# Optimization experiments

Hardware: AMD Instinct MI355X
Metric: run time of the kernel (lower is better)

The kernel has to match this reference:

```python
import jax, jax.numpy as jnp
import numpy as np
from jax import lax

WIN_SIZE = 11
SIGMA = 1.5
WEIGHTS = jnp.array([0.0448, 0.2856, 0.3001, 0.2363, 0.1333], dtype=jnp.float32)
C1 = (0.01 * 1.0) ** 2  # val_range = 1.0
C2 = (0.03 * 1.0) ** 2


def gaussian_kernel2d(kernel_size, sigma):
    g = jnp.arange(kernel_size, dtype=jnp.float32) - kernel_size // 2
    g = jnp.exp(-(g ** 2) / (2.0 * sigma ** 2))
    g = g / g.sum()
    return jnp.outer(g, g)  # [k, k]


def depthwise_conv(x, k2d):
    # x: [B, C, H, W]; same gaussian window applied per-channel (groups=C), VALID padding
    C = x.shape[1]
    w = jnp.broadcast_to(k2d, (C, 1) + k2d.shape).astype(x.dtype)
    return lax.conv_general_dilated(x, w, (1, 1), 'VALID',
                                    feature_group_count=C,
                                    dimension_numbers=('NCHW', 'OIHW', 'NCHW'))


def ssim_index(x, y, k2d, nonnegative=True):
    # returns (ss, cs) each of shape [B, C] (spatial mean, per channel)
    m1 = depthwise_conv(x, k2d)
    m2 = depthwise_conv(y, k2d)
    m12 = m1 * m2
    m1s = m1 * m1
    m2s = m2 * m2
    v1 = depthwise_conv(x * x, k2d) - m1s
    v2 = depthwise_conv(y * y, k2d) - m2s
    cov = depthwise_conv(x * y, k2d) - m12
    cs = (2.0 * cov + C2) / (v1 + v2 + C2)
    ss = (2.0 * m12 + C1) / (m1s + m2s + C1) * cs
    ss = ss.reshape(ss.shape[0], ss.shape[1], -1).mean(axis=-1)
    cs = cs.reshape(cs.shape[0], cs.shape[1], -1).mean(axis=-1)
    if nonnegative:
        ss = jnp.maximum(ss, 0.0)
        cs = jnp.maximum(cs, 0.0)
    return ss, cs


def avg_pool2(x):
    # F.avg_pool2d(kernel_size=2). Input spatial dims are even at every scale
    # (512 -> 32), so ceil_mode never pads; plain 2x2/2 mean pooling is exact.
    s = lax.reduce_window(x, jnp.array(0.0, x.dtype), lax.add,
                          (1, 1, 2, 2), (1, 1, 2, 2), 'VALID')
    return s * 0.25


def setup_inputs() -> dict:
    key = jax.random.key(0)
    k1, k2 = jax.random.split(key)
    B, C, H, W = 4, 12, 512, 512
    pred = jax.random.normal(k1, (B, C, H, W), dtype=jnp.float32)
    target = jax.random.randint(k2, (B, H, W), 0, C, dtype=jnp.int64)
    return {"pred": pred, "target": target}


def reference(pred, target):
    # MS_SSIMLoss.forward with process_input=True, nonnegative=True.
    # The per-class python loop in the original is an independent depthwise
    # computation per channel -> vectorized here as a C-channel grouped conv;
    # loss = mean over classes of (1 - mean over batch of msss) == 1 - mean(msss).
    num_classes = pred.shape[1]
    x = jax.nn.softmax(pred, axis=1)
    y = jax.nn.one_hot(target, num_classes, dtype=pred.dtype).transpose(0, 3, 1, 2)
    k2d = gaussian_kernel2d(WIN_SIZE, SIGMA)
    m = WEIGHTS.shape[0]
    vals = []
    for i in range(m):
        if i > 0:
            x = avg_pool2(x)
            y = avg_pool2(y)
        ss, cs = ssim_index(x, y, k2d, nonnegative=True)
        vals.append(cs if i + 1 < m else ss)
    stacked = jnp.stack(vals, axis=-1)  # [B, C, m]
    msss = jnp.prod(stacked ** WEIGHTS, axis=-1)  # [B, C]
    return 1.0 - msss.mean()
```

## Files before the change

### kernel.cpp

```cpp
#include <hip/hip_runtime.h>

#define NCH 12
#define NB  4
#define BC  48
#define HW0 (512 * 512)

#define GK_INIT { 0.00102840f, 0.00759863f, 0.03600078f, 0.10936081f, \
                  0.21300541f, 0.26601164f, 0.21300541f, 0.10936081f, \
                  0.03600078f, 0.00759863f, 0.00102840f }

__global__ void k_denom(const float4* __restrict__ pred, float4* __restrict__ U,
                        double* __restrict__ acc) {
    if (blockIdx.x == 0) {
        for (int t = threadIdx.x; t < 480; t += 256) acc[t] = 0.0;
    }
    int i = blockIdx.x * blockDim.x + threadIdx.x;
    if (i >= NB * (HW0 / 4)) return;
    int b = i >> 16;
    int p = i & 65535;
    const float4* base = pred + (((size_t)b * NCH) << 16) + p;
    float4 s = make_float4(0.f, 0.f, 0.f, 0.f);
#pragma unroll
    for (int c = 0; c < NCH; ++c) {
        float4 v = base[(size_t)c << 16];
        s.x += expf(v.x); s.y += expf(v.y);
        s.z += expf(v.z); s.w += expf(v.w);
    }
    float4 u;
    u.x = 1.f / s.x; u.y = 1.f / s.y; u.z = 1.f / s.z; u.w = 1.f / s.w;
    U[((size_t)b << 16) + p] = u;
}

__global__ __launch_bounds__(256, 8)
void k_ssim0(const float* __restrict__ pred, const float* __restrict__ U,
             const int* __restrict__ tgt, double* __restrict__ acc,
             float* __restrict__ Xp, unsigned short* __restrict__ Yp) {
    constexpr int SS = 43;
    constexpr int TS = 35;
    constexpr int H = 512, W = 512, OH = 502, OW = 502, tilesX = 16;
    __shared__ float sx[42 * SS + 4];
    __shared__ uint2 tm4[42 * TS];
    __shared__ unsigned long long ybits[30];
    __shared__ float red[8];

    const float gk[11] = GK_INIT;

    const int bc = blockIdx.y;
    const int tile = blockIdx.x;
    const int ty = tile / tilesX, tx = tile - ty * tilesX;
    const int oy = ty * 32, ox = tx * 32;
    const int tid = threadIdx.x;
    const bool interior = (oy + 41 < H) && (ox + 41 < W);

    const int b = bc / NCH, cls = bc - (bc / NCH) * NCH;
    const float* Pb = pred + (((size_t)b * NCH + cls) << 18);
    const float* Ub = U + ((size_t)b << 18);
    const int* Tb = tgt + ((size_t)b << 18);

    {
        int r = tid / 42, c = tid - (tid / 42) * 42;
#pragma unroll
        for (int k = 0; k < 7; ++k) {
            bool inr = (k < 6) || (tid < 228);
            int gy = oy + r, gx = ox + c;
            bool ld = inr && (interior || (gy < H && gx < W));
            float xv = 0.f;
            bool bit = false;
            if (ld) {
                int off = gy * W + gx;
                xv = expf(Pb[off]) * Ub[off];
                bit = (Tb[off] == cls);
            }
            unsigned long long mk = __ballot(bit);
            if ((tid & 63) == 0) ybits[(tid >> 6) + (k << 2)] = mk;
            if (inr) sx[r * SS + c] = xv;
            c += 4; r += 6;
            if (c >= 42) { c -= 42; r += 1; }
        }
        if (tid == 0) { ybits[28] = 0ull; ybits[29] = 0ull; }
    }
    __syncthreads();

    if (tid < 252) {
        int rr = tid / 6, s = tid - (tid / 6) * 6;
        int c0 = s * 6;
        const float* px = sx + rr * SS + c0;
        float ac0[6] = {}, ac1[6] = {}, ac2[6] = {}, ac3[6] = {};
        unsigned long long win;
        {
            int i0 = rr * 42 + c0;
            int w = i0 >> 6, sh = i0 & 63;
            unsigned long long lo = ybits[w], hi = ybits[w + 1];
            win = sh ? ((lo >> sh) | (hi << (64 - sh))) : lo;
        }
#pragma unroll
        for (int j = 0; j < 16; ++j) {
            float xv = px[j];
            float xx = xv * xv;
            bool bit = (win >> j) & 1;
            float yv = bit ? 1.f : 0.f;
            float xy = bit ? xv : 0.f;
#pragma unroll
            for (int o = 0; o < 6; ++o) {
                int kk = j - o;
                if (kk >= 0 && kk <= 10) {
                    float g = gk[kk];
                    ac0[o] = fmaf(g, xv, ac0[o]);
                    ac1[o] = fmaf(g, yv, ac1[o]);
                    ac2[o] = fmaf(g, xx, ac2[o]);
                    ac3[o] = fmaf(g, xy, ac3[o]);
                }
            }
        }
        int ob = rr * TS + c0;
#pragma unroll
        for (int o = 0; o < 6; ++o) {
            if (c0 + o < 32) {
                unsigned ua = __float_as_uint(ac0[o]);
                unsigned ub = __float_as_uint(ac1[o]);
                unsigned uc = __float_as_uint(ac2[o]);
                unsigned ud = __float_as_uint(ac3[o]);
                tm4[ob + o] = make_uint2((ua >> 16) | (ub & 0xFFFF0000u),
                                         (uc >> 16) | (ud & 0xFFFF0000u));
            }
        }
    }
    __syncthreads();

    const float C1 = 1e-4f, C2 = 9e-4f;
    const int cc = tid & 31, rg = tid >> 5, r0 = rg << 2;
    float a0[4] = {}, a1[4] = {}, a2[4] = {}, a3[4] = {};
    const int vb = r0 * TS + cc;
#pragma unroll
    for (int k = 0; k < 14; ++k) {
        uint2 tv = tm4[vb + k * TS];
        float m1v = __uint_as_float(tv.x << 16);
        float m2v = __uint_as_float(tv.x & 0xFFFF0000u);
        float xxv = __uint_as_float(tv.y << 16);
        float xyv = __uint_as_float(tv.y & 0xFFFF0000u);
#pragma unroll
        for (int j = 0; j < 4; ++j) {
            int kk = k - j;
            if (kk >= 0 && kk <= 10) {
                float g = gk[kk];
                a0[j] = fmaf(g, m1v, a0[j]);
                a1[j] = fmaf(g, m2v, a1[j]);
                a2[j] = fmaf(g, xxv, a2[j]);
                a3[j] = fmaf(g, xyv, a3[j]);
            }
        }
    }
    float cs_l = 0.f, ss_l = 0.f;
    const bool colok = (ox + cc < OW);
#pragma unroll
    for (int j = 0; j < 4; ++j) {
        if (colok && (oy + r0 + j < OH)) {
            float m1 = a0[j], m2 = a1[j];
            float sxx = a2[j], sxy_ = a3[j];
            float m11 = m1 * m1, m22 = m2 * m2, m12 = m1 * m2;
            float v1 = sxx - m11, v2 = m2 - m22, cov = sxy_ - m12;
            float d1 = m11 + m22 + C1, d2 = v1 + v2 + C2;
            float n2 = 2.f * cov + C2;
            float q = 1.f / (d1 * d2);
            cs_l = fmaf(n2 * d1, q, cs_l);
            ss_l = fmaf((2.f * m12 + C1) * n2, q, ss_l);
        }
    }

    {
        int py = tid >> 4, pxx = tid & 15;
        int s0 = (py * 2) * SS + pxx * 2;
        float xs = 0.25f * (sx[s0] + sx[s0 + 1] + sx[s0 + SS] + sx[s0 + SS + 1]);
        size_t oidx = ((size_t)bc * 256 + (oy >> 1) + py) * 256 + (ox >> 1) + pxx;
        Xp[oidx] = xs;
        int i0 = (py * 2) * 42 + pxx * 2, i1 = i0 + 42;
        unsigned c0 = (unsigned)((ybits[i0 >> 6] >> (i0 & 63)) & 1ull);
        unsigned c1 = (unsigned)((ybits[(i0 + 1) >> 6] >> ((i0 + 1) & 63)) & 1ull);
        unsigned c2 = (unsigned)((ybits[i1 >> 6] >> (i1 & 63)) & 1ull);
        unsigned c3 = (unsigned)((ybits[(i1 + 1) >> 6] >> ((i1 + 1) & 63)) & 1ull);
        Yp[oidx] = (unsigned short)((c0 + c1 + c2 + c3) << 6);
    }

    for (int off = 32; off; off >>= 1) {
        cs_l += __shfl_down(cs_l, off);
        ss_l += __shfl_down(ss_l, off);
    }
    int wv = tid >> 6, ln = tid & 63;
    if (ln == 0) { red[wv] = cs_l; red[4 + wv] = ss_l; }
    __syncthreads();
    if (tid == 0) {
        double cs_b = (double)red[0] + (double)red[1] + (double)red[2] + (double)red[3];
        double ss_b = (double)red[4] + (double)red[5] + (double)red[6] + (double)red[7];
        atomicAdd(&acc[bc], cs_b);
        atomicAdd(&acc[48 + bc], ss_b);
    }
}

template <int PIN>
__device__ __forceinline__ void ssim_tile_g(
    const float* __restrict__ Xs, const unsigned short* __restrict__ Ys,
    int H, int W, int OH, int OW, int tilesX, int tile, int bc,
    double* __restrict__ acc, int scale,
    float* sx, float4* tm4, float* tm5, unsigned short* syu, float* red) {
    constexpr int SS = 43;
    constexpr int TS = 35;
    const float gk[11] = GK_INIT;

    const int ty = tile / tilesX, tx = tile - ty * tilesX;
    const int oy = ty * 32, ox = tx * 32;
    const int tid = threadIdx.x;
    const bool interior = (oy + 41 < H) && (ox + 41 < W);

    constexpr int SC = 1 << PIN;
    const int SW = W * SC;
    const float* Xb = Xs + (size_t)bc * H * W * SC * SC;
    const unsigned short* Yb = Ys + (size_t)bc * H * W * SC * SC;

    {
        int r = tid / 42, c = tid - (tid / 42) * 42;
#pragma unroll
        for (int k = 0; k < 7; ++k) {
            bool inr = (k < 6) || (tid < 228);
            int gy = oy + r, gx = ox + c;
            bool ld = inr && (interior || (gy < H && gx < W));
            float xv = 0.f;
            unsigned short yv = 0;
            if (ld) {
                if constexpr (PIN == 0) {
                    int off = gy * SW + gx;
                    xv = Xb[off];
                    yv = Yb[off];
                } else {
                    const float* q = Xb + (SC * gy) * SW + SC * gx;
                    const unsigned short* qy = Yb + (SC * gy) * SW + SC * gx;
                    float s = 0.f; unsigned us = 0;
#pragma unroll
                    for (int a = 0; a < SC; ++a) {
#pragma unroll
                        for (int e = 0; e < SC; ++e) {
                            s += q[a * SW + e];
                            us += qy[a * SW + e];
                        }
                    }
                    xv = s * (1.f / (float)(SC * SC));
                    yv = (unsigned short)(us >> (2 * PIN));
                }
            }
            if (inr) { sx[r * SS + c] = xv; syu[r * SS + c] = yv; }
            c += 4; r += 6;
            if (c >= 42) { c -= 42; r += 1; }
        }
    }
    __syncthreads();

    if (tid < 252) {
        int rr = tid / 6, s = tid - (tid / 6) * 6;
        int c0 = s * 6;
        const float* px = sx + rr * SS + c0;
        const unsigned short* pyu = syu + rr * SS + c0;
        float ac0[6] = {}, ac1[6] = {}, ac2[6] = {}, ac3[6] = {}, ac4[6] = {};
#pragma unroll
        for (int j = 0; j < 16; ++j) {
            float xv = px[j];
            float xx = xv * xv;
            float yv = (float)pyu[j];
            float xy = xv * yv;
            float yy = yv * yv;
#pragma unroll
            for (int o = 0; o < 6; ++o) {
                int kk = j - o;
                if (kk >= 0 && kk <= 10) {
                    float g = gk[kk];
                    ac0[o] = fmaf(g, xv, ac0[o]);
                    ac1[o] = fmaf(g, yv, ac1[o]);
                    ac2[o] = fmaf(g, xx, ac2[o]);
                    ac3[o] = fmaf(g, xy, ac3[o]);
                    ac4[o] = fmaf(g, yy, ac4[o]);
                }
            }
        }
        int ob = rr * TS + c0;
#pragma unroll
        for (int o = 0; o < 6; ++o) {
            if (c0 + o < 32) {
                tm4[ob + o] = make_float4(ac0[o], ac1[o], ac2[o], ac3[o]);
                tm5[ob + o] = ac4[o];
            }
        }
    }
    __syncthreads();

    const float C1 = 1e-4f, C2 = 9e-4f;
    const int cc = tid & 31, rg = tid >> 5, r0 = rg << 2;
    float a0[4] = {}, a1[4] = {}, a2[4] = {}, a3[4] = {}, a4[4] = {};
    const int vb = r0 * TS + cc;
#pragma unroll
    for (int k = 0; k < 14; ++k) {
        float4 tv = tm4[vb + k * TS];
        float t4 = tm5[vb + k * TS];
#pragma unroll
        for (int j = 0; j < 4; ++j) {
            int kk = k - j;
            if (kk >= 0 && kk <= 10) {
                float g = gk[kk];
                a0[j] = fmaf(g, tv.x, a0[j]);
                a1[j] = fmaf(g, tv.y, a1[j]);
                a2[j] = fmaf(g, tv.z, a2[j]);
                a3[j] = fmaf(g, tv.w, a3[j]);
                a4[j] = fmaf(g, t4, a4[j]);
            }
        }
    }
    float cs_l = 0.f, ss_l = 0.f;
    const bool colok = (ox + cc < OW);
#pragma unroll
    for (int j = 0; j < 4; ++j) {
        if (colok && (oy + r0 + j < OH)) {
            float m1 = a0[j];
            float m2 = a1[j] * (1.f / 256.f);
            float sxx = a2[j];
            float sxy_ = a3[j] * (1.f / 256.f);
            float syy_ = a4[j] * (1.f / 65536.f);
            float m11 = m1 * m1, m22 = m2 * m2, m12 = m1 * m2;
            float v1 = sxx - m11, v2 = syy_ - m22, cov = sxy_ - m12;
            float d1 = m11 + m22 + C1, d2 = v1 + v2 + C2;
            float n2 = 2.f * cov + C2;
            float q = 1.f / (d1 * d2);
            cs_l = fmaf(n2 * d1, q, cs_l);
            ss_l = fmaf((2.f * m12 + C1) * n2, q, ss_l);
        }
    }

    for (int offs = 32; offs; offs >>= 1) {
        cs_l += __shfl_down(cs_l, offs);
        ss_l += __shfl_down(ss_l, offs);
    }
    int wv = tid >> 6, ln = tid & 63;
    if (ln == 0) { red[wv] = cs_l; red[4 + wv] = ss_l; }
    __syncthreads();
    if (tid == 0) {
        double cs_b = (double)red[0] + (double)red[1] + (double)red[2] + (double)red[3];
        double ss_b = (double)red[4] + (double)red[5] + (double)red[6] + (double)red[7];
        atomicAdd(&acc[scale * 96 + bc], cs_b);
        atomicAdd(&acc[scale * 96 + 48 + bc], ss_b);
    }
}

__global__ __launch_bounds__(256, 4)
void k_rest(const float* __restrict__ X1, const unsigned short* __restrict__ Y1,
            double* __restrict__ acc) {
    __shared__ float sx[42 * 43 + 4];
    __shared__ float4 tm4[42 * 35];
    __shared__ float tm5[42 * 35];
    __shared__ unsigned short syu[42 * 43 + 4];
    __shared__ float red[8];
    const int gb = blockIdx.x;

    if (gb < 3072) {
        ssim_tile_g<0>(X1, Y1, 256, 256, 246, 246, 8, gb & 63, gb >> 6,
                       acc, 1, sx, tm4, tm5, syu, red);
    } else if (gb < 3840) {
        int t = gb - 3072;
        ssim_tile_g<1>(X1, Y1, 128, 128, 118, 118, 4, t & 15, t >> 4,
                       acc, 2, sx, tm4, tm5, syu, red);
    } else if (gb < 4032) {
        int t = gb - 3840;
        ssim_tile_g<2>(X1, Y1, 64, 64, 54, 54, 2, t & 3, t >> 2,
                       acc, 3, sx, tm4, tm5, syu, red);
    } else {
        ssim_tile_g<3>(X1, Y1, 32, 32, 22, 22, 1, 0, gb - 4032,
                       acc, 4, sx, tm4, tm5, syu, red);
    }
}

__global__ void k_final(const double* __restrict__ acc, float* __restrict__ out) {
    const float wts[5] = {0.0448f, 0.2856f, 0.3001f, 0.2363f, 0.1333f};
    const float cnt[5] = {252004.f, 60516.f, 13924.f, 2916.f, 484.f};
    int tid = threadIdx.x;
    float msss = 0.f;
    if (tid < BC) {
        msss = 1.f;
#pragma unroll
        for (int s = 0; s < 5; ++s) {
            double a = (s < 4) ? acc[s * 96 + tid] : acc[s * 96 + 48 + tid];
            float v = fmaxf((float)(a / (double)cnt[s]), 0.f);
            msss *= powf(v, wts[s]);
        }
    }
    for (int off = 32; off; off >>= 1) msss += __shfl_down(msss, off);
    if (tid == 0) out[0] = 1.f - msss * (1.f / (float)BC);
}

extern "C" void kernel_launch(void* const* d_in, const int* in_sizes, int n_in,
                              void* d_out, int out_size, void* d_ws, size_t ws_size,
                              hipStream_t stream) {
    const float* pred = (const float*)d_in[0];
    const int*   tgt  = (const int*)d_in[1];
    float* out = (float*)d_out;

    double* acc = (double*)d_ws;
    float* U  = (float*)(acc + 480);
    float* X1 = U + (size_t)NB * 512 * 512;
    unsigned short* Y1 = (unsigned short*)(X1 + (size_t)BC * 256 * 256);

    k_denom<<<(NB * (HW0 / 4) + 255) / 256, 256, 0, stream>>>(
        (const float4*)pred, (float4*)U, acc);

    k_ssim0<<<dim3(256, BC), 256, 0, stream>>>(pred, U, tgt, acc, X1, Y1);

    k_rest<<<dim3(4080), 256, 0, stream>>>(X1, Y1, acc);

    k_final<<<1, 64, 0, stream>>>(acc, out);
}
```

Baseline: 251.8 us.

## Store horizontal-pass intermediates as truncated bf16 in shared memory, use fast exp

The horizontal Gaussian pass results in k_rest are truncated to their upper 16 bits (bf16) and packed, which shrinks the LDS intermediate arrays so more blocks fit per CU (launch bounds raised to 6 waves-per-block occupancy). expf is replaced by __expf in the softmax kernels. Truncating the intermediates loses precision in the variance and covariance terms, where a small difference is taken between two nearly equal values. That could push the SSIM results past tolerance.

```diff
diff --git a/kernel.cpp b/kernel.cpp
--- a/kernel.cpp
+++ b/kernel.cpp
@@ -23,8 +23,8 @@
 #pragma unroll
     for (int c = 0; c < NCH; ++c) {
         float4 v = base[(size_t)c << 16];
-        s.x += expf(v.x); s.y += expf(v.y);
-        s.z += expf(v.z); s.w += expf(v.w);
+        s.x += __expf(v.x); s.y += __expf(v.y);
+        s.z += __expf(v.z); s.w += __expf(v.w);
     }
     float4 u;
     u.x = 1.f / s.x; u.y = 1.f / s.y; u.z = 1.f / s.z; u.w = 1.f / s.w;
@@ -68,7 +68,7 @@
             bool bit = false;
             if (ld) {
                 int off = gy * W + gx;
-                xv = expf(Pb[off]) * Ub[off];
+                xv = __expf(Pb[off]) * Ub[off];
                 bit = (Tb[off] == cls);
             }
             unsigned long long mk = __ballot(bit);
@@ -201,7 +201,7 @@
     const float* __restrict__ Xs, const unsigned short* __restrict__ Ys,
     int H, int W, int OH, int OW, int tilesX, int tile, int bc,
     double* __restrict__ acc, int scale,
-    float* sx, float4* tm4, float* tm5, unsigned short* syu, float* red) {
+    float* sx, uint2* tm4, unsigned short* tm5, unsigned short* syu, float* red) {
     constexpr int SS = 43;
     constexpr int TS = 35;
     const float gk[11] = GK_INIT;
@@ -283,8 +283,13 @@
 #pragma unroll
         for (int o = 0; o < 6; ++o) {
             if (c0 + o < 32) {
-                tm4[ob + o] = make_float4(ac0[o], ac1[o], ac2[o], ac3[o]);
-                tm5[ob + o] = ac4[o];
+                unsigned ua = __float_as_uint(ac0[o]);
+                unsigned ub = __float_as_uint(ac1[o]);
+                unsigned uc = __float_as_uint(ac2[o]);
+                unsigned ud = __float_as_uint(ac3[o]);
+                tm4[ob + o] = make_uint2((ua >> 16) | (ub & 0xFFFF0000u),
+                                         (uc >> 16) | (ud & 0xFFFF0000u));
+                tm5[ob + o] = (unsigned short)(__float_as_uint(ac4[o]) >> 16);
             }
         }
     }
@@ -296,18 +301,22 @@
     const int vb = r0 * TS + cc;
 #pragma unroll
     for (int k = 0; k < 14; ++k) {
-        float4 tv = tm4[vb + k * TS];
-        float t4 = tm5[vb + k * TS];
+        uint2 tv = tm4[vb + k * TS];
+        float m1v = __uint_as_float(tv.x << 16);
+        float m2v = __uint_as_float(tv.x & 0xFFFF0000u);
+        float xxv = __uint_as_float(tv.y << 16);
+        float xyv = __uint_as_float(tv.y & 0xFFFF0000u);
+        float yyv = __uint_as_float((unsigned)tm5[vb + k * TS] << 16);
 #pragma unroll
         for (int j = 0; j < 4; ++j) {
             int kk = k - j;
             if (kk >= 0 && kk <= 10) {
                 float g = gk[kk];
-                a0[j] = fmaf(g, tv.x, a0[j]);
-                a1[j] = fmaf(g, tv.y, a1[j]);
-                a2[j] = fmaf(g, tv.z, a2[j]);
-                a3[j] = fmaf(g, tv.w, a3[j]);
-                a4[j] = fmaf(g, t4, a4[j]);
+                a0[j] = fmaf(g, m1v, a0[j]);
+                a1[j] = fmaf(g, m2v, a1[j]);
+                a2[j] = fmaf(g, xxv, a2[j]);
+                a3[j] = fmaf(g, xyv, a3[j]);
+                a4[j] = fmaf(g, yyv, a4[j]);
             }
         }
     }
@@ -346,12 +355,12 @@
     }
 }
 
-__global__ __launch_bounds__(256, 4)
+__global__ __launch_bounds__(256, 6)
 void k_rest(const float* __restrict__ X1, const unsigned short* __restrict__ Y1,
             double* __restrict__ acc) {
     __shared__ float sx[42 * 43 + 4];
-    __shared__ float4 tm4[42 * 35];
-    __shared__ float tm5[42 * 35];
+    __shared__ uint2 tm4[42 * 35];
+    __shared__ unsigned short tm5[42 * 35];
     __shared__ unsigned short syu[42 * 43 + 4];
     __shared__ float red[8];
     const int gb = blockIdx.x;
```

Result: slower. 265.6 us (+5.5%).
